# Optimization experiments

Hardware: AMD Instinct MI355X
Metric: run time of the kernel (lower is better)

Reference implementation:

```python
import jax, jax.numpy as jnp
import numpy as np

NEG_SLOPE = 0.2  # PyG GATConv default negative_slope


def gat_layer(x, W, a_src, a_dst, bias, src, dst, num_nodes):
    # x: [N, Fin], W: [Fin, H*C], a_src/a_dst: [H, C], bias: [C]
    H, C = a_src.shape
    h = (x @ W).reshape(num_nodes, H, C)                      # [N, H, C]
    alpha_src = jnp.einsum('nhc,hc->nh', h, a_src)            # [N, H]
    alpha_dst = jnp.einsum('nhc,hc->nh', h, a_dst)            # [N, H]
    e = jax.nn.leaky_relu(alpha_src[src] + alpha_dst[dst], NEG_SLOPE)  # [E, H]
    # segment softmax over incoming edges of each destination node
    m = jax.ops.segment_max(e, dst, num_segments=num_nodes)  # [N, H]
    p = jnp.exp(e - m[dst])
    denom = jax.ops.segment_sum(p, dst, num_segments=num_nodes)
    alpha = p / denom[dst]                                    # [E, H]
    out = jax.ops.segment_sum(h[src] * alpha[:, :, None], dst,
                              num_segments=num_nodes)         # [N, H, C]
    return out.mean(axis=1) + bias                            # concat=False -> mean


def setup_inputs() -> dict:
    key = jax.random.key(0)
    ks = jax.random.split(key, 8)
    N, E, F, H = 20000, 640000, 128, 4
    s = 0.1  # weight init scale
    return {
        'x': jax.random.normal(ks[0], (N, F), jnp.float32),
        'W1': jax.random.normal(ks[1], (F, H * F), jnp.float32) * s,
        'a_src1': jax.random.normal(ks[2], (H, F), jnp.float32) * s,
        'a_dst1': jax.random.normal(ks[3], (H, F), jnp.float32) * s,
        'b1': jnp.zeros((F,), jnp.float32),
        'W2': jax.random.normal(ks[4], (F, F), jnp.float32) * s,
        'a_src2': jax.random.normal(ks[5], (1, F), jnp.float32) * s,
        'a_dst2': jax.random.normal(ks[6], (1, F), jnp.float32) * s,
        'b2': jnp.zeros((F,), jnp.float32),
        'edge_index': jax.random.randint(ks[7], (2, E), 0, N, jnp.int32),
    }


def reference(x, W1, a_src1, a_dst1, b1, W2, a_src2, a_dst2, b2, edge_index):
    N = x.shape[0]
    loop = jnp.arange(N, dtype=edge_index.dtype)  # add_self_loops=True (PyG default)
    src = jnp.concatenate([edge_index[0], loop])
    dst = jnp.concatenate([edge_index[1], loop])
    h = jax.nn.elu(gat_layer(x, W1, a_src1, a_dst1, b1, src, dst, N))
    out = jax.nn.elu(gat_layer(h, W2, a_src2, a_dst2, b2, src, dst, N))
    return out
```

## Files before the change

kernel.cpp:

```cpp
#include <hip/hip_runtime.h>
#include <hip/hip_bf16.h>


typedef short v8s __attribute__((ext_vector_type(8)));
typedef float v4f __attribute__((ext_vector_type(4)));
typedef float v2f __attribute__((ext_vector_type(2)));

template <int K> struct IC { static constexpr int value = K; };

constexpr int MAXD = 128;
constexpr int EPB = 4096;
constexpr int BINW = 64;

__device__ __forceinline__ void bf2x(unsigned int u, float& lo, float& hi) {
    union { unsigned int i; float f; } a, b;
    a.i = u << 16;
    b.i = u & 0xffff0000u;
    lo = a.f;
    hi = b.f;
}
__device__ __forceinline__ v2f bf2p(unsigned int u) {
    union { unsigned int i; float f; } a, b;
    a.i = u << 16;
    b.i = u & 0xffff0000u;
    return (v2f){a.f, b.f};
}
__device__ __forceinline__ unsigned short f2bf(float f) {
    union { float f; unsigned int i; } v;
    v.f = f;
    unsigned int lsb = (v.i >> 16) & 1u;
    v.i += 0x7fffu + lsb;
    return (unsigned short)(v.i >> 16);
}
__device__ __forceinline__ unsigned int pack2(float a, float b) {
    return (unsigned int)f2bf(a) | ((unsigned int)f2bf(b) << 16);
}

__device__ __forceinline__ void scan512_incl(unsigned int* a, int tid) {
#pragma unroll
    for (int off = 1; off < 512; off <<= 1) {
        unsigned int v0 = (tid >= off) ? a[tid - off] : 0u;
        unsigned int v1 = a[tid + 256 - off];
        __syncthreads();
        a[tid] += v0;
        a[tid + 256] += v1;
        __syncthreads();
    }
}

__global__ void fused_prep_kernel(const float* __restrict__ x,
                                  const float* __restrict__ W1, const float* __restrict__ W2,
                                  const float* __restrict__ as1v, const float* __restrict__ ad1v,
                                  const float* __restrict__ as2v, const float* __restrict__ ad2v,
                                  unsigned short* __restrict__ xb,
                                  unsigned short* __restrict__ Bt1,
                                  unsigned short* __restrict__ Bt2,
                                  float* __restrict__ wsrc1, float* __restrict__ wdst1,
                                  float* __restrict__ wsrc2, float* __restrict__ wdst2,
                                  unsigned int* __restrict__ ghist,
                                  unsigned int* __restrict__ bincur,
                                  float* __restrict__ as2, float* __restrict__ ad2,
                                  int N, int NB) {
    const int Bcast = (N * 32 + 255) / 256;
    int b = blockIdx.x;
    if (b < Bcast) {
        int i = (b * 256 + threadIdx.x) * 4;
        if (i + 3 < N * 128) {
            float4 v = *(const float4*)&x[i];
            ushort4 o;
            o.x = f2bf(v.x);
            o.y = f2bf(v.y);
            o.z = f2bf(v.z);
            o.w = f2bf(v.w);
            *(ushort4*)&xb[i] = o;
        } else {
            for (; i < N * 128; ++i) xb[i] = f2bf(x[i]);
        }
        return;
    }
    b -= Bcast;
    if (b < 256) {
        int i = b * 256 + threadIdx.x;
        int c = i >> 9;
        int r = i & 511;
        int h = r >> 7, k = r & 127;
        Bt1[i] = f2bf(W1[(size_t)k * 512 + (h << 7) + c] * 0.25f);
        return;
    }
    b -= 256;
    if (b < 64) {
        int i = b * 256 + threadIdx.x;
        int c = i >> 7, k = i & 127;
        Bt2[i] = f2bf(W2[(size_t)k * 128 + c]);
        return;
    }
    b -= 64;
    if (b < 2) {
        int i = b * 256 + threadIdx.x;
        int h = i >> 7, k = i & 127;
        const float* wr = W1 + (size_t)k * 512 + (h << 7);
        const float* as_ = as1v + (h << 7);
        const float* ad_ = ad1v + (h << 7);
        float s1 = 0.f, s2 = 0.f;
        for (int c = 0; c < 128; ++c) {
            float wv = wr[c];
            s1 += wv * as_[c];
            s2 += wv * ad_[c];
        }
        wsrc1[i] = s1;
        wdst1[i] = s2;
        return;
    }
    b -= 2;
    if (b < 1) {
        int k = threadIdx.x;
        if (k < 128) {
            const float* wr = W2 + (size_t)k * 128;
            float s1 = 0.f, s2 = 0.f;
            for (int c = 0; c < 128; ++c) {
                float wv = wr[c];
                s1 += wv * as2v[c];
                s2 += wv * ad2v[c];
            }
            wsrc2[k] = s1;
            wdst2[k] = s2;
        }
        return;
    }
    b -= 1;
    {
        int i = b * 256 + threadIdx.x;
        if (i < N) {
            as2[i] = 0.f;
            ad2[i] = 0.f;
        }
        if (i < NB) {
            ghist[i] = 0u;
            bincur[i] = 0u;
        }
    }
}

__launch_bounds__(256)
__global__ void hist_alpha_kernel(const int* __restrict__ dst, int E,
                                  unsigned int* __restrict__ ghist, int NB, int Bh,
                                  const unsigned int* __restrict__ xrow,
                                  const float* __restrict__ wsrc, const float* __restrict__ wdst,
                                  float* __restrict__ asrc, float* __restrict__ adst, int N) {
    if ((int)blockIdx.x < Bh) {
        __shared__ unsigned int bh[512];
        const int tid = threadIdx.x;
        bh[tid] = 0u;
        bh[tid + 256] = 0u;
        __syncthreads();
        const int e0 = blockIdx.x * EPB;
        const int ne = min(EPB, E - e0);
#pragma unroll
        for (int k = 0; k < 4; ++k) {
            int rel = (k * 256 + tid) * 4;
            if (rel < ne) {
                int4 d4 = *(const int4*)&dst[e0 + rel];
                atomicAdd(&bh[(unsigned int)d4.x >> 6], 1u);
                atomicAdd(&bh[(unsigned int)d4.y >> 6], 1u);
                atomicAdd(&bh[(unsigned int)d4.z >> 6], 1u);
                atomicAdd(&bh[(unsigned int)d4.w >> 6], 1u);
            }
        }
        __syncthreads();
        unsigned int c0 = bh[tid], c1 = bh[tid + 256];
        if (tid < NB && c0) atomicAdd(&ghist[tid], c0);
        if (tid + 256 < NB && c1) atomicAdd(&ghist[tid + 256], c1);
        return;
    }
    constexpr int H = 4;
    __shared__ float s_wv[2 * H * 128];
    for (int i = threadIdx.x; i < 2 * H * 128; i += 256)
        s_wv[i] = (i < H * 128) ? wsrc[i] : wdst[i - H * 128];
    __syncthreads();
    const int wid = threadIdx.x >> 6, lane = threadIdx.x & 63;
    const int n = (blockIdx.x - Bh) * 4 + wid;
    if (n >= N) return;
    unsigned int u = xrow[(size_t)n * 64 + lane];
    float f0, f1;
    bf2x(u, f0, f1);
    float s1[H], s2[H];
#pragma unroll
    for (int h = 0; h < H; ++h) {
        float2 ws = *(const float2*)&s_wv[h * 128 + 2 * lane];
        float2 wd = *(const float2*)&s_wv[H * 128 + h * 128 + 2 * lane];
        s1[h] = f0 * ws.x + f1 * ws.y;
        s2[h] = f0 * wd.x + f1 * wd.y;
    }
#pragma unroll
    for (int off = 32; off; off >>= 1)
#pragma unroll
        for (int h = 0; h < H; ++h) {
            s1[h] += __shfl_xor(s1[h], off);
            s2[h] += __shfl_xor(s2[h], off);
        }
    if (lane == 0) {
#pragma unroll
        for (int h = 0; h < H; ++h) {
            asrc[(size_t)n * H + h] = s1[h];
            adst[(size_t)n * H + h] = s2[h];
        }
    }
}

__launch_bounds__(256)
__global__ void csr_partition_kernel(const int* __restrict__ src, const int* __restrict__ dst,
                                     const unsigned int* __restrict__ ghist,
                                     unsigned int* __restrict__ bincur,
                                     unsigned int* __restrict__ binBuf, int E, int NB) {
    __shared__ unsigned int bh[512];
    __shared__ unsigned int g[512];
    __shared__ unsigned int sres[512];
    __shared__ unsigned int stg[EPB];
    const int tid = threadIdx.x;
    const int e0 = blockIdx.x * EPB;
    const int ne = min(EPB, E - e0);
    bh[tid] = 0u;
    bh[tid + 256] = 0u;
    g[tid] = (tid < NB) ? ghist[tid] : 0u;
    g[tid + 256] = (tid + 256 < NB) ? ghist[tid + 256] : 0u;
    __syncthreads();

    unsigned int pk[16], ps[16];
#pragma unroll
    for (int k = 0; k < 4; ++k) {
        int rel = (k * 256 + tid) * 4;
        if (rel < ne) {
            int4 s4 = *(const int4*)&src[e0 + rel];
            int4 d4 = *(const int4*)&dst[e0 + rel];
            int ss[4] = {s4.x, s4.y, s4.z, s4.w};
            int dd[4] = {d4.x, d4.y, d4.z, d4.w};
#pragma unroll
            for (int j = 0; j < 4; ++j) {
                unsigned int bin = (unsigned int)dd[j] >> 6;
                pk[k * 4 + j] = (unsigned int)ss[j] |
                                (((unsigned int)dd[j] & 63u) << 15) | (bin << 21);
                ps[k * 4 + j] = atomicAdd(&bh[bin], 1u);
            }
        } else {
#pragma unroll
            for (int j = 0; j < 4; ++j) pk[k * 4 + j] = 0xffffffffu;
        }
    }
    __syncthreads();
    unsigned int c0 = bh[tid], c1 = bh[tid + 256];
    unsigned int r0 = 0u, r1 = 0u;
    if (tid < NB && c0) r0 = atomicAdd(&bincur[tid], c0);
    if (tid + 256 < NB && c1) r1 = atomicAdd(&bincur[tid + 256], c1);
    sres[tid] = r0;
    sres[tid + 256] = r1;
    __syncthreads();
    scan512_incl(bh, tid);
    scan512_incl(g, tid);
#pragma unroll
    for (int k = 0; k < 16; ++k) {
        unsigned int p = pk[k];
        if (p != 0xffffffffu) {
            unsigned int bin = p >> 21;
            unsigned int lo = bin ? bh[bin - 1] : 0u;
            stg[lo + ps[k]] = p;
        }
    }
    __syncthreads();
    for (int j = tid; j < ne; j += 256) {
        unsigned int p = stg[j];
        unsigned int bin = p >> 21;
        unsigned int gst = bin ? g[bin - 1] : 0u;
        unsigned int lo = bin ? bh[bin - 1] : 0u;
        binBuf[gst + sres[bin] + (unsigned int)j - lo] = p;
    }
}

__launch_bounds__(256)
__global__ void csr_build_kernel(const unsigned int* __restrict__ ghist,
                                 const unsigned int* __restrict__ binBuf,
                                 unsigned short* __restrict__ slot,
                                 int* __restrict__ cnt, int N, int NB) {
    __shared__ unsigned int g[512];
    __shared__ unsigned int scnt[BINW];
    __shared__ unsigned short sslot[BINW][MAXD];
    const int tid = threadIdx.x;
    const int b = blockIdx.x;
    g[tid] = (tid < NB) ? ghist[tid] : 0u;
    g[tid + 256] = (tid + 256 < NB) ? ghist[tid + 256] : 0u;
    if (tid < BINW) {
        scnt[tid] = 1u;
        sslot[tid][0] = (unsigned short)(b * BINW + tid);
    }
    __syncthreads();
    scan512_incl(g, tid);
    const unsigned int lo = b ? g[b - 1] : 0u;
    const unsigned int hiE = g[b];
    for (unsigned int j = lo + tid; j < hiE; j += 256) {
        unsigned int p = binBuf[j];
        int dl = (int)((p >> 15) & 63u);
        unsigned int pos = atomicAdd(&scnt[dl], 1u);
        if (pos < (unsigned int)MAXD) sslot[dl][pos] = (unsigned short)(p & 0x7fffu);
    }
    __syncthreads();
    const int rows = min(BINW, N - b * BINW);
    const int nq = rows * (MAXD / 8);
    uint4* gdst = (uint4*)(slot + (size_t)b * BINW * MAXD);
    const uint4* lsrc = (const uint4*)&sslot[0][0];
    for (int j = tid; j < nq; j += 256) gdst[j] = lsrc[j];
    if (tid < rows) cnt[b * BINW + tid] = (int)min(scnt[tid], (unsigned int)MAXD);
}

template <int H, int NPB>
__launch_bounds__(64 * NPB, 4)
__global__ void gat_gather_kernel(const uint4* __restrict__ xrow4,
                                  const float* __restrict__ asrc,
                                  const float* __restrict__ adst,
                                  const int* __restrict__ cnt,
                                  const unsigned short* __restrict__ slot,
                                  uint4* __restrict__ Sb4,
                                  int N) {
    static_assert(H == 4 || H == 1, "H");
    const int wid = threadIdx.x >> 6, lane = threadIdx.x & 63;
    const int q = lane >> 4, l16 = lane & 15;
    const int n = blockIdx.x * NPB + wid;
    if (n >= N) return;

    __shared__ int s_src_all[NPB][64];
    __shared__ float s_w_all[NPB][64 * H];
    int* s_src = s_src_all[wid];
    float* s_w = s_w_all[wid];

    const int base = n * MAXD;
    const int deg = min(cnt[n], MAXD);

    float adst_n[H];
#pragma unroll
    for (int h = 0; h < H; ++h) adst_n[h] = adst[(size_t)n * H + h];

    float sum_h[H] = {};
    v2f acc[4 * H];
#pragma unroll
    for (int i = 0; i < 4 * H; ++i) acc[i] = (v2f){0.f, 0.f};

    auto do_batch = [&](int j0, auto kc) {
        constexpr int KK = decltype(kc)::value;
        int ss[KK];
        uint4 d[KK];
#pragma unroll
        for (int k = 0; k < KK; ++k) ss[k] = s_src[j0 + k * 4 + q];
#pragma unroll
        for (int k = 0; k < KK; ++k) d[k] = xrow4[(size_t)ss[k] * 16 + l16];
#pragma unroll
        for (int k = 0; k < KK; ++k) {
            v2f f2[4];
            f2[0] = bf2p(d[k].x);
            f2[1] = bf2p(d[k].y);
            f2[2] = bf2p(d[k].z);
            f2[3] = bf2p(d[k].w);
            if constexpr (H == 4) {
                float4 w = *(const float4*)&s_w[(j0 + k * 4 + q) * 4];
                v2f w0 = (v2f){w.x, w.x}, w1 = (v2f){w.y, w.y};
                v2f w2 = (v2f){w.z, w.z}, w3 = (v2f){w.w, w.w};
#pragma unroll
                for (int j = 0; j < 4; ++j) {
                    acc[j] += w0 * f2[j];
                    acc[4 + j] += w1 * f2[j];
                    acc[8 + j] += w2 * f2[j];
                    acc[12 + j] += w3 * f2[j];
                }
            } else {
                float w = s_w[j0 + k * 4 + q];
                v2f w0 = (v2f){w, w};
#pragma unroll
                for (int j = 0; j < 4; ++j) acc[j] += w0 * f2[j];
            }
        }
    };

    for (int i0 = 0; i0 < deg; i0 += 64) {
        const int cntc = min(64, deg - i0);
        {
            const bool valid = lane < cntc;
            int idx = i0 + (valid ? lane : (cntc - 1));
            int s = (int)slot[base + idx];
            s_src[lane] = s;
            if constexpr (H == 4) {
                float4 av = ((const float4*)asrc)[s];
                float ev[4] = {av.x, av.y, av.z, av.w};
#pragma unroll
                for (int hh = 0; hh < 4; ++hh) {
                    float e = ev[hh] + adst_n[hh];
                    e = e > 0.f ? e : 0.2f * e;
                    float wv = valid ? __expf(e) : 0.f;
                    s_w[lane * 4 + hh] = wv;
                    sum_h[hh] += wv;
                }
            } else {
                float e = asrc[s] + adst_n[0];
                e = e > 0.f ? e : 0.2f * e;
                float wv = valid ? __expf(e) : 0.f;
                s_w[lane] = wv;
                sum_h[0] += wv;
            }
        }
        __threadfence_block();

        int j0 = 0;
        for (; j0 + 32 <= cntc; j0 += 32) do_batch(j0, IC<8>{});
        const int rem = cntc - j0;
        if (rem > 0) {
            switch ((rem + 3) >> 2) {
                case 1: do_batch(j0, IC<1>{}); break;
                case 2: do_batch(j0, IC<2>{}); break;
                case 3: do_batch(j0, IC<3>{}); break;
                case 4: do_batch(j0, IC<4>{}); break;
                case 5: do_batch(j0, IC<5>{}); break;
                case 6: do_batch(j0, IC<6>{}); break;
                case 7: do_batch(j0, IC<7>{}); break;
                default: do_batch(j0, IC<8>{}); break;
            }
        }
    }

#pragma unroll
    for (int i = 0; i < 4 * H; ++i) {
        acc[i][0] += __shfl_xor(acc[i][0], 16);
        acc[i][1] += __shfl_xor(acc[i][1], 16);
        acc[i][0] += __shfl_xor(acc[i][0], 32);
        acc[i][1] += __shfl_xor(acc[i][1], 32);
    }
#pragma unroll
    for (int off = 32; off; off >>= 1)
#pragma unroll
        for (int h = 0; h < H; ++h) sum_h[h] += __shfl_xor(sum_h[h], off);

    if constexpr (H == 4) {
#pragma unroll
        for (int h = 0; h < 4; ++h) {
            if (q == h) {
                float rd = 1.0f / sum_h[h];
                uint4 o;
                o.x = pack2(acc[h * 4 + 0][0] * rd, acc[h * 4 + 0][1] * rd);
                o.y = pack2(acc[h * 4 + 1][0] * rd, acc[h * 4 + 1][1] * rd);
                o.z = pack2(acc[h * 4 + 2][0] * rd, acc[h * 4 + 2][1] * rd);
                o.w = pack2(acc[h * 4 + 3][0] * rd, acc[h * 4 + 3][1] * rd);
                Sb4[(size_t)n * 64 + h * 16 + l16] = o;
            }
        }
    } else {
        if (q == 0) {
            float rd = 1.0f / sum_h[0];
            uint4 o;
            o.x = pack2(acc[0][0] * rd, acc[0][1] * rd);
            o.y = pack2(acc[1][0] * rd, acc[1][1] * rd);
            o.z = pack2(acc[2][0] * rd, acc[2][1] * rd);
            o.w = pack2(acc[3][0] * rd, acc[3][1] * rd);
            Sb4[(size_t)n * 16 + l16] = o;
        }
    }
}

__device__ __forceinline__ void store_out(float* p, float v) { *p = v; }
__device__ __forceinline__ void store_out(unsigned short* p, float v) { *p = f2bf(v); }

template <typename OT, bool ELU, bool FUSE_A2>
__launch_bounds__(256)
__global__ void gemm_bias_act_kernel(const unsigned short* __restrict__ A,
                                     const unsigned short* __restrict__ Bt,
                                     const float* __restrict__ bias,
                                     OT* __restrict__ C,
                                     const float* __restrict__ ws2,
                                     const float* __restrict__ wd2,
                                     float* __restrict__ as2, float* __restrict__ ad2,
                                     int M, int Nout, int K) {
    constexpr int BK = 32;
    __shared__ unsigned short As[64][40];
    __shared__ unsigned short Bs[64][40];

    const int tid = threadIdx.x;
    const int w = tid >> 6;
    const int lane = tid & 63;
    const int m16 = lane & 15;
    const int kg = lane >> 4;
    const int m0 = blockIdx.y * 64;
    const int n0 = blockIdx.x * 64;

    v4f acc[4];
#pragma unroll
    for (int i = 0; i < 4; ++i) acc[i] = (v4f){0.f, 0.f, 0.f, 0.f};

    const int srow = tid >> 2;
    const int sseg = tid & 3;
    const int arow_g = min(m0 + srow, M - 1);
    const unsigned short* Ap = &A[(size_t)arow_g * K + sseg * 8];
    const unsigned short* Bp = &Bt[(size_t)(n0 + srow) * K + sseg * 8];

    for (int k0 = 0; k0 < K; k0 += BK) {
        uint4 av = *(const uint4*)(Ap + k0);
        uint4 bv = *(const uint4*)(Bp + k0);
        __syncthreads();
        *(uint4*)&As[srow][sseg * 8] = av;
        *(uint4*)&Bs[srow][sseg * 8] = bv;
        __syncthreads();
        v8s a = *(const v8s*)&As[w * 16 + m16][kg * 8];
#pragma unroll
        for (int i = 0; i < 4; ++i) {
            v8s b = *(const v8s*)&Bs[i * 16 + m16][kg * 8];
            acc[i] = __builtin_amdgcn_mfma_f32_16x16x32_bf16(a, b, acc[i], 0, 0, 0);
        }
    }

    float pr_s[4] = {}, pr_d[4] = {};
#pragma unroll
    for (int i = 0; i < 4; ++i) {
        const int col = n0 + i * 16 + m16;
        const float bv = bias[col];
        float w2s = 0.f, w2d = 0.f;
        if constexpr (FUSE_A2) {
            w2s = ws2[col];
            w2d = wd2[col];
        }
#pragma unroll
        for (int r = 0; r < 4; ++r) {
            int row = m0 + w * 16 + kg * 4 + r;
            if (row < M) {
                float val = acc[i][r] + bv;
                if constexpr (ELU) val = val > 0.f ? val : (__expf(val) - 1.0f);
                store_out(&C[(size_t)row * Nout + col], val);
                if constexpr (FUSE_A2) {
                    pr_s[r] += val * w2s;
                    pr_d[r] += val * w2d;
                }
            }
        }
    }
    if constexpr (FUSE_A2) {
#pragma unroll
        for (int off = 1; off < 16; off <<= 1)
#pragma unroll
            for (int r = 0; r < 4; ++r) {
                pr_s[r] += __shfl_xor(pr_s[r], off);
                pr_d[r] += __shfl_xor(pr_d[r], off);
            }
        if (m16 == 0) {
#pragma unroll
            for (int r = 0; r < 4; ++r) {
                int row = m0 + w * 16 + kg * 4 + r;
                if (row < M) {
                    atomicAdd(&as2[row], pr_s[r]);
                    atomicAdd(&ad2[row], pr_d[r]);
                }
            }
        }
    }
}


extern "C" void kernel_launch(void* const* d_in, const int* in_sizes, int n_in,
                              void* d_out, int out_size, void* d_ws, size_t ws_size,
                              hipStream_t stream) {
    const float* x = (const float*)d_in[0];
    const float* W1 = (const float*)d_in[1];
    const float* a_src1 = (const float*)d_in[2];
    const float* a_dst1 = (const float*)d_in[3];
    const float* b1 = (const float*)d_in[4];
    const float* W2 = (const float*)d_in[5];
    const float* a_src2 = (const float*)d_in[6];
    const float* a_dst2 = (const float*)d_in[7];
    const float* b2 = (const float*)d_in[8];
    const int* edge = (const int*)d_in[9];
    float* out = (float*)d_out;

    constexpr int F = 128, H = 4;
    const int N = in_sizes[0] / F;
    const int E = in_sizes[9] / 2;
    const int NB = (N + BINW - 1) / BINW;

    char* ws = (char*)d_ws;
    size_t o = 0;
    auto take = [&](size_t bytes) {
        char* p = ws + o;
        o = (o + bytes + 255) & ~(size_t)255;
        return p;
    };
    int* cnt = (int*)take((size_t)N * 4);
    unsigned short* slot = (unsigned short*)take((size_t)N * MAXD * 2);
    unsigned int* ghist = (unsigned int*)take((size_t)NB * 4);
    unsigned int* bincur = (unsigned int*)take((size_t)NB * 4);
    unsigned int* binBuf = (unsigned int*)take((size_t)E * 4);
    unsigned short* xb = (unsigned short*)take((size_t)N * F * 2);
    unsigned short* Bt1 = (unsigned short*)take((size_t)F * H * F * 2);
    unsigned short* Bt2 = (unsigned short*)take((size_t)F * F * 2);
    float* wsrc1 = (float*)take((size_t)H * F * 4);
    float* wdst1 = (float*)take((size_t)H * F * 4);
    float* wsrc2 = (float*)take((size_t)F * 4);
    float* wdst2 = (float*)take((size_t)F * 4);
    float* as1 = (float*)take((size_t)N * H * 4);
    float* ad1 = (float*)take((size_t)N * H * 4);
    unsigned short* Sb1 = (unsigned short*)take((size_t)N * H * F * 2);
    unsigned short* h2b = (unsigned short*)take((size_t)N * F * 2);
    float* as2 = (float*)take((size_t)N * 4);
    float* ad2 = (float*)take((size_t)N * 4);
    unsigned short* S2b = (unsigned short*)take((size_t)N * F * 2);
    (void)ws_size;

    const int* esrc = edge;
    const int* edst = edge + E;

    const int Bcast = (N * 32 + 255) / 256;
    const int Bzero = (N + 255) / 256;
    hipLaunchKernelGGL(fused_prep_kernel, dim3(Bcast + 256 + 64 + 2 + 1 + Bzero), dim3(256), 0,
                       stream, x, W1, W2, a_src1, a_dst1, a_src2, a_dst2, xb, Bt1, Bt2, wsrc1,
                       wdst1, wsrc2, wdst2, ghist, bincur, as2, ad2, N, NB);

    const int Bh = (E + EPB - 1) / EPB;
    const int Balpha = (N + 3) / 4;
    hipLaunchKernelGGL(hist_alpha_kernel, dim3(Bh + Balpha), dim3(256), 0, stream, edst, E,
                       ghist, NB, Bh, (const unsigned int*)xb, wsrc1, wdst1, as1, ad1, N);

    hipLaunchKernelGGL(csr_partition_kernel, dim3(Bh), dim3(256), 0, stream, esrc, edst, ghist,
                       bincur, binBuf, E, NB);
    hipLaunchKernelGGL(csr_build_kernel, dim3(NB), dim3(256), 0, stream, ghist, binBuf, slot,
                       cnt, N, NB);

    hipLaunchKernelGGL((gat_gather_kernel<H, 4>), dim3((N + 3) / 4), dim3(256), 0, stream,
                       (const uint4*)xb, as1, ad1, cnt, slot, (uint4*)Sb1, N);
    hipLaunchKernelGGL((gemm_bias_act_kernel<unsigned short, true, true>),
                       dim3(F / 64, (N + 63) / 64), dim3(256), 0, stream, Sb1, Bt1, b1, h2b,
                       wsrc2, wdst2, as2, ad2, N, F, H * F);

    hipLaunchKernelGGL((gat_gather_kernel<1, 4>), dim3((N + 3) / 4), dim3(256), 0, stream,
                       (const uint4*)h2b, as2, ad2, cnt, slot, (uint4*)S2b, N);
    hipLaunchKernelGGL((gemm_bias_act_kernel<float, true, false>), dim3(F / 64, (N + 63) / 64),
                       dim3(256), 0, stream, S2b, Bt2, b2, out, nullptr, nullptr, nullptr,
                       nullptr, N, F, F);
}
```

Measured before the change: 197.6 us.

## Replace global histogram partition with per-block local bucketing and offsets

Drops the separate global histogram pass and the csr_partition kernel. Each edge block now bucket-sorts its edges locally in shared memory, writes them contiguously, and records per-bin inclusive offsets as 16-bit values. The build kernel then walks every block's segment for its bin instead of reading one contiguous global range. This removes one launch, the second read of the edge arrays, and the global atomics. In exchange, each build block makes about 157 small scattered reads per bin and has threads loop serially over segments.

```diff
diff --git a/kernel.cpp b/kernel.cpp
--- a/kernel.cpp
+++ b/kernel.cpp
@@ -57,10 +57,7 @@
                                   unsigned short* __restrict__ Bt2,
                                   float* __restrict__ wsrc1, float* __restrict__ wdst1,
                                   float* __restrict__ wsrc2, float* __restrict__ wdst2,
-                                  unsigned int* __restrict__ ghist,
-                                  unsigned int* __restrict__ bincur,
-                                  float* __restrict__ as2, float* __restrict__ ad2,
-                                  int N, int NB) {
+                                  float* __restrict__ as2, float* __restrict__ ad2, int N) {
     const int Bcast = (N * 32 + 255) / 256;
     int b = blockIdx.x;
     if (b < Bcast) {
@@ -134,42 +131,65 @@
             as2[i] = 0.f;
             ad2[i] = 0.f;
         }
-        if (i < NB) {
-            ghist[i] = 0u;
-            bincur[i] = 0u;
-        }
     }
 }
 
 __launch_bounds__(256)
-__global__ void hist_alpha_kernel(const int* __restrict__ dst, int E,
-                                  unsigned int* __restrict__ ghist, int NB, int Bh,
+__global__ void part_alpha_kernel(const int* __restrict__ src, const int* __restrict__ dst,
+                                  int E, unsigned int* __restrict__ binBuf,
+                                  unsigned short* __restrict__ boff,
+                                  int Bh,
                                   const unsigned int* __restrict__ xrow,
                                   const float* __restrict__ wsrc, const float* __restrict__ wdst,
                                   float* __restrict__ asrc, float* __restrict__ adst, int N) {
     if ((int)blockIdx.x < Bh) {
         __shared__ unsigned int bh[512];
+        __shared__ unsigned int stg[EPB];
         const int tid = threadIdx.x;
         bh[tid] = 0u;
         bh[tid + 256] = 0u;
         __syncthreads();
         const int e0 = blockIdx.x * EPB;
         const int ne = min(EPB, E - e0);
+
+        unsigned int pk[16], ps[16];
 #pragma unroll
         for (int k = 0; k < 4; ++k) {
             int rel = (k * 256 + tid) * 4;
             if (rel < ne) {
+                int4 s4 = *(const int4*)&src[e0 + rel];
                 int4 d4 = *(const int4*)&dst[e0 + rel];
-                atomicAdd(&bh[(unsigned int)d4.x >> 6], 1u);
-                atomicAdd(&bh[(unsigned int)d4.y >> 6], 1u);
-                atomicAdd(&bh[(unsigned int)d4.z >> 6], 1u);
-                atomicAdd(&bh[(unsigned int)d4.w >> 6], 1u);
-            }
-        }
-        __syncthreads();
-        unsigned int c0 = bh[tid], c1 = bh[tid + 256];
-        if (tid < NB && c0) atomicAdd(&ghist[tid], c0);
-        if (tid + 256 < NB && c1) atomicAdd(&ghist[tid + 256], c1);
+                int ss[4] = {s4.x, s4.y, s4.z, s4.w};
+                int dd[4] = {d4.x, d4.y, d4.z, d4.w};
+#pragma unroll
+                for (int j = 0; j < 4; ++j) {
+                    unsigned int bin = (unsigned int)dd[j] >> 6;
+                    pk[k * 4 + j] = (unsigned int)ss[j] |
+                                    (((unsigned int)dd[j] & 63u) << 15) | (bin << 21);
+                    ps[k * 4 + j] = atomicAdd(&bh[bin], 1u);
+                }
+            } else {
+#pragma unroll
+                for (int j = 0; j < 4; ++j) pk[k * 4 + j] = 0xffffffffu;
+            }
+        }
+        __syncthreads();
+        scan512_incl(bh, tid);
+#pragma unroll
+        for (int k = 0; k < 16; ++k) {
+            unsigned int p = pk[k];
+            if (p != 0xffffffffu) {
+                unsigned int bin = p >> 21;
+                unsigned int lo = bin ? bh[bin - 1] : 0u;
+                stg[lo + ps[k]] = p;
+            }
+        }
+        __syncthreads();
+        unsigned int* out = binBuf + (size_t)blockIdx.x * EPB;
+        for (int j = tid; j < ne; j += 256) out[j] = stg[j];
+        unsigned short* bo = boff + (size_t)blockIdx.x * 512;
+        bo[tid] = (unsigned short)bh[tid];
+        bo[tid + 256] = (unsigned short)bh[tid + 256];
         return;
     }
     constexpr int H = 4;
@@ -208,98 +228,30 @@
 }
 
 __launch_bounds__(256)
-__global__ void csr_partition_kernel(const int* __restrict__ src, const int* __restrict__ dst,
-                                     const unsigned int* __restrict__ ghist,
-                                     unsigned int* __restrict__ bincur,
-                                     unsigned int* __restrict__ binBuf, int E, int NB) {
-    __shared__ unsigned int bh[512];
-    __shared__ unsigned int g[512];
-    __shared__ unsigned int sres[512];
-    __shared__ unsigned int stg[EPB];
-    const int tid = threadIdx.x;
-    const int e0 = blockIdx.x * EPB;
-    const int ne = min(EPB, E - e0);
-    bh[tid] = 0u;
-    bh[tid + 256] = 0u;
-    g[tid] = (tid < NB) ? ghist[tid] : 0u;
-    g[tid + 256] = (tid + 256 < NB) ? ghist[tid + 256] : 0u;
-    __syncthreads();
-
-    unsigned int pk[16], ps[16];
-#pragma unroll
-    for (int k = 0; k < 4; ++k) {
-        int rel = (k * 256 + tid) * 4;
-        if (rel < ne) {
-            int4 s4 = *(const int4*)&src[e0 + rel];
-            int4 d4 = *(const int4*)&dst[e0 + rel];
-            int ss[4] = {s4.x, s4.y, s4.z, s4.w};
-            int dd[4] = {d4.x, d4.y, d4.z, d4.w};
-#pragma unroll
-            for (int j = 0; j < 4; ++j) {
-                unsigned int bin = (unsigned int)dd[j] >> 6;
-                pk[k * 4 + j] = (unsigned int)ss[j] |
-                                (((unsigned int)dd[j] & 63u) << 15) | (bin << 21);
-                ps[k * 4 + j] = atomicAdd(&bh[bin], 1u);
-            }
-        } else {
-#pragma unroll
-            for (int j = 0; j < 4; ++j) pk[k * 4 + j] = 0xffffffffu;
-        }
-    }
-    __syncthreads();
-    unsigned int c0 = bh[tid], c1 = bh[tid + 256];
-    unsigned int r0 = 0u, r1 = 0u;
-    if (tid < NB && c0) r0 = atomicAdd(&bincur[tid], c0);
-    if (tid + 256 < NB && c1) r1 = atomicAdd(&bincur[tid + 256], c1);
-    sres[tid] = r0;
-    sres[tid + 256] = r1;
-    __syncthreads();
-    scan512_incl(bh, tid);
-    scan512_incl(g, tid);
-#pragma unroll
-    for (int k = 0; k < 16; ++k) {
-        unsigned int p = pk[k];
-        if (p != 0xffffffffu) {
-            unsigned int bin = p >> 21;
-            unsigned int lo = bin ? bh[bin - 1] : 0u;
-            stg[lo + ps[k]] = p;
-        }
-    }
-    __syncthreads();
-    for (int j = tid; j < ne; j += 256) {
-        unsigned int p = stg[j];
-        unsigned int bin = p >> 21;
-        unsigned int gst = bin ? g[bin - 1] : 0u;
-        unsigned int lo = bin ? bh[bin - 1] : 0u;
-        binBuf[gst + sres[bin] + (unsigned int)j - lo] = p;
-    }
-}
-
-__launch_bounds__(256)
-__global__ void csr_build_kernel(const unsigned int* __restrict__ ghist,
-                                 const unsigned int* __restrict__ binBuf,
+__global__ void csr_build_kernel(const unsigned int* __restrict__ binBuf,
+                                 const unsigned short* __restrict__ boff,
                                  unsigned short* __restrict__ slot,
-                                 int* __restrict__ cnt, int N, int NB) {
-    __shared__ unsigned int g[512];
+                                 int* __restrict__ cnt, int N, int Bh) {
     __shared__ unsigned int scnt[BINW];
     __shared__ unsigned short sslot[BINW][MAXD];
     const int tid = threadIdx.x;
     const int b = blockIdx.x;
-    g[tid] = (tid < NB) ? ghist[tid] : 0u;
-    g[tid + 256] = (tid + 256 < NB) ? ghist[tid + 256] : 0u;
     if (tid < BINW) {
         scnt[tid] = 1u;
         sslot[tid][0] = (unsigned short)(b * BINW + tid);
     }
     __syncthreads();
-    scan512_incl(g, tid);
-    const unsigned int lo = b ? g[b - 1] : 0u;
-    const unsigned int hiE = g[b];
-    for (unsigned int j = lo + tid; j < hiE; j += 256) {
-        unsigned int p = binBuf[j];
-        int dl = (int)((p >> 15) & 63u);
-        unsigned int pos = atomicAdd(&scnt[dl], 1u);
-        if (pos < (unsigned int)MAXD) sslot[dl][pos] = (unsigned short)(p & 0x7fffu);
+    for (int k = tid; k < Bh; k += 256) {
+        const unsigned short* bo = boff + (size_t)k * 512;
+        unsigned int lo = b ? (unsigned int)bo[b - 1] : 0u;
+        unsigned int hi = (unsigned int)bo[b];
+        const unsigned int* buf = binBuf + (size_t)k * EPB;
+        for (unsigned int j = lo; j < hi; ++j) {
+            unsigned int p = buf[j];
+            int dl = (int)((p >> 15) & 63u);
+            unsigned int pos = atomicAdd(&scnt[dl], 1u);
+            if (pos < (unsigned int)MAXD) sslot[dl][pos] = (unsigned short)(p & 0x7fffu);
+        }
     }
     __syncthreads();
     const int rows = min(BINW, N - b * BINW);
@@ -574,7 +526,7 @@
     constexpr int F = 128, H = 4;
     const int N = in_sizes[0] / F;
     const int E = in_sizes[9] / 2;
-    const int NB = (N + BINW - 1) / BINW;
+    const int Bh = (E + EPB - 1) / EPB;
 
     char* ws = (char*)d_ws;
     size_t o = 0;
@@ -585,9 +537,8 @@
     };
     int* cnt = (int*)take((size_t)N * 4);
     unsigned short* slot = (unsigned short*)take((size_t)N * MAXD * 2);
-    unsigned int* ghist = (unsigned int*)take((size_t)NB * 4);
-    unsigned int* bincur = (unsigned int*)take((size_t)NB * 4);
-    unsigned int* binBuf = (unsigned int*)take((size_t)E * 4);
+    unsigned int* binBuf = (unsigned int*)take((size_t)Bh * EPB * 4);
+    unsigned short* boff = (unsigned short*)take((size_t)Bh * 512 * 2);
     unsigned short* xb = (unsigned short*)take((size_t)N * F * 2);
     unsigned short* Bt1 = (unsigned short*)take((size_t)F * H * F * 2);
     unsigned short* Bt2 = (unsigned short*)take((size_t)F * F * 2);
@@ -611,17 +562,15 @@
     const int Bzero = (N + 255) / 256;
     hipLaunchKernelGGL(fused_prep_kernel, dim3(Bcast + 256 + 64 + 2 + 1 + Bzero), dim3(256), 0,
                        stream, x, W1, W2, a_src1, a_dst1, a_src2, a_dst2, xb, Bt1, Bt2, wsrc1,
-                       wdst1, wsrc2, wdst2, ghist, bincur, as2, ad2, N, NB);
-
-    const int Bh = (E + EPB - 1) / EPB;
+                       wdst1, wsrc2, wdst2, as2, ad2, N);
+
     const int Balpha = (N + 3) / 4;
-    hipLaunchKernelGGL(hist_alpha_kernel, dim3(Bh + Balpha), dim3(256), 0, stream, edst, E,
-                       ghist, NB, Bh, (const unsigned int*)xb, wsrc1, wdst1, as1, ad1, N);
-
-    hipLaunchKernelGGL(csr_partition_kernel, dim3(Bh), dim3(256), 0, stream, esrc, edst, ghist,
-                       bincur, binBuf, E, NB);
-    hipLaunchKernelGGL(csr_build_kernel, dim3(NB), dim3(256), 0, stream, ghist, binBuf, slot,
-                       cnt, N, NB);
+    hipLaunchKernelGGL(part_alpha_kernel, dim3(Bh + Balpha), dim3(256), 0, stream, esrc, edst,
+                       E, binBuf, boff, Bh, (const unsigned int*)xb, wsrc1, wdst1, as1, ad1, N);
+
+    const int NB = (N + BINW - 1) / BINW;
+    hipLaunchKernelGGL(csr_build_kernel, dim3(NB), dim3(256), 0, stream, binBuf, boff, slot,
+                       cnt, N, Bh);
 
     hipLaunchKernelGGL((gat_gather_kernel<H, 4>), dim3((N + 3) / 4), dim3(256), 0, stream,
                        (const uint4*)xb, as1, ad1, cnt, slot, (uint4*)Sb1, N);
```

Result: faster. 190.6 us (-3.5%).
